# Kernel optimization log

Measured on AMD Instinct MI355X. Metric: run time of the kernel, lower is better.

Reference implementation:

```python
import jax, jax.numpy as jnp
import numpy as np

# Config mirrors TACO_hashed init: data_size=[1024,1024], dimensions=[[4]*5,[4]*5]
N = 262144          # number of query coordinates
DH = 256            # dim_hidden
TD = 4              # tile_dim = dimensions[0][0]
NLEV = 5            # n_levels
W0C = 30.0          # w0
DIMS = np.array([[4]*NLEV, [4]*NLEV])                 # [2, n_levels]
CUM = 1024 // np.cumprod(DIMS, axis=1)                # cum_bases per axis, [2, n_levels]


def setup_inputs() -> dict:
    key = jax.random.key(0)
    ks = jax.random.split(key, 9)
    s = 1.0 / np.sqrt(DH)
    e = TD * TD  # embedding dim = tile_dim**2 = 16
    return {
        "coords": jax.random.randint(ks[0], (N, 2), 0, 1024, dtype=jnp.int32),
        "W0": jax.random.normal(ks[1], (2, DH), jnp.float32) * (1.0 / np.sqrt(2.0)),
        "b0": jnp.zeros((DH,), jnp.float32),
        "Wh": jax.random.normal(ks[2], (3, DH, DH), jnp.float32) * s,  # hidden SIREN linears
        "bh": jnp.zeros((3, DH), jnp.float32),
        "emb": jax.random.normal(ks[3], (NLEV - 1, e, e), jnp.float32),      # per-level embedding tables
        "modW": jax.random.normal(ks[4], (NLEV - 1, e, DH), jnp.float32) * (1.0 / np.sqrt(e)),  # modulator linears (no bias)
        "Wl": jax.random.normal(ks[5], (DH, 3), jnp.float32) * s,  # last_layer
        "bl": jnp.zeros((3,), jnp.float32),
    }


def reference(coords, W0, b0, Wh, bh, emb, modW, Wl, bl):
    dims = jnp.asarray(DIMS.T)   # [n_levels, 2]
    cum = jnp.asarray(CUM.T)     # [n_levels, 2]
    # decompose_coords: per-level bitwise-style div/mod  -> [N, n_levels, 2]
    lv = (coords[:, None, :] // cum[None]) % dims[None]
    # modulator indices for levels 1..n_levels-1: idx = y*tile_dim + x  -> [N, n_levels-1]
    idx = lv[:, 1:, 1] * TD + lv[:, 1:, 0]
    # SIREN input is level-0 coords as float (faithful to the source)
    x = lv[:, 0, :].astype(jnp.float32) @ W0 + b0
    x = x + W0C * (emb[0][idx[:, 0]] @ modW[0])
    x = jnp.sin(W0C * x)
    for j in range(3):
        x = x @ Wh[j] + bh[j]
        x = x + W0C * (emb[j + 1][idx[:, j + 1]] @ modW[j + 1])
        x = jnp.sin(W0C * x)
    return x @ Wl + bl
```

## Files before the change

kernel.cpp:

```cpp
#include <hip/hip_runtime.h>
#include <hip/hip_bf16.h>
#include <math.h>


typedef float  f32x4  __attribute__((ext_vector_type(4)));
typedef int    i32x4  __attribute__((ext_vector_type(4)));
typedef __bf16 bf16x8 __attribute__((ext_vector_type(8)));

__device__ __forceinline__ float fbar(float v) {
  asm volatile("" : "+v"(v));
  return v;
}

__device__ __forceinline__ unsigned short f2bf_rne(float x) {
  unsigned u = __float_as_uint(x);
  unsigned r = (u + 0x7fffu + ((u >> 16) & 1u)) >> 16;
  return (unsigned short)r;
}

__device__ __forceinline__ void gload16(const void* g, void* l) {
  __builtin_amdgcn_global_load_lds(
      (const __attribute__((address_space(1))) unsigned*)g,
      (__attribute__((address_space(3))) unsigned*)l, 16, 0, 0);
}

__device__ __forceinline__ void sincos30(float x, float* so, float* co) {
  const float Ch = 4.774648189544678f;
  const float Cl = 1.0321218e-07f;
  float revh = x * Ch;
  fbar(revh);
  float e    = __builtin_fmaf(x, Ch, -revh);
  float revl = __builtin_fmaf(x, Cl, e);
  float k2   = __builtin_rintf(revh + revh);
  float g    = __builtin_fmaf(k2, -0.5f, revh) + revl;
  float u = g * g;
  float sr = -15.0946f;
  sr = __builtin_fmaf(sr, u, 42.0601f);
  sr = __builtin_fmaf(sr, u, -76.70585f);
  sr = __builtin_fmaf(sr, u, 81.6052492f);
  sr = __builtin_fmaf(sr, u, -41.341702f);
  sr = __builtin_fmaf(sr, u, 6.2831853f);
  float s = g * sr;
  float cr = -26.4259f;
  cr = __builtin_fmaf(cr, u, 60.2446f);
  cr = __builtin_fmaf(cr, u, -85.4568f);
  cr = __builtin_fmaf(cr, u, 64.9393940f);
  cr = __builtin_fmaf(cr, u, -19.7392088f);
  float c = __builtin_fmaf(cr, u, 1.0f);
  int ki = (int)k2;
  unsigned sgn = ((unsigned)(ki & 1)) << 31;
  *so = __uint_as_float(__float_as_uint(s) ^ sgn);
  *co = __uint_as_float(__float_as_uint(c) ^ sgn);
}

__global__ void k_prep(const float* __restrict__ emb, const float* __restrict__ modW,
                       float* __restrict__ Mf, float* __restrict__ T2C,
                       float* __restrict__ T2S, const float* __restrict__ Wl,
                       unsigned* __restrict__ B2u, const float* __restrict__ W2,
                       unsigned short* __restrict__ B2T) {
  int b = blockIdx.x, d = threadIdx.x;
  if (b < 64) {
    int j = b >> 4, i = b & 15;
    float acc = 0.0f;
#pragma unroll
    for (int e = 0; e < 16; ++e)
      acc = __builtin_fmaf(emb[j * 256 + i * 16 + e], modW[(j * 16 + e) * 256 + d], acc);
    Mf[b * 256 + d] = acc;
    if (j == 2) {
      float pm = fbar(30.0f * acc);
      float s, c;
      sincos30(pm, &s, &c);
      T2C[i * 256 + d] = c;
      T2S[i * 256 + d] = s;
    } else if (j == 3) {
      float pm = fbar(30.0f * acc);
      float s, c;
      sincos30(pm, &s, &c);
#pragma unroll
      for (int q = 0; q < 3; ++q) {
        float w = Wl[d * 3 + q];
        unsigned ts = (unsigned)f2bf_rne(s * w);
        unsigned tc = (unsigned)f2bf_rne(c * w);
        B2u[(i * 3 + q) * 256 + d] = (tc << 16) | ts;
      }
    }
  } else {
    int col = b - 64, k = d;
    float w = W2[k * 256 + col];
    unsigned short hi = f2bf_rne(w);
    float hif = __uint_as_float((unsigned)hi << 16);
    unsigned short lo = f2bf_rne(w - hif);
    B2T[col * 768 + k] = hi;
    B2T[col * 768 + 256 + k] = lo;
    B2T[col * 768 + 512 + k] = hi;
  }
}

__global__ void __launch_bounds__(512) k_h123(
    const float* __restrict__ W0, const float* __restrict__ b0,
    const float* __restrict__ Wh0, const float* __restrict__ bh0,
    const float* __restrict__ W1, const float* __restrict__ b1,
    const float* __restrict__ Mf, const float* __restrict__ T2C,
    const float* __restrict__ T2S,
    unsigned short* __restrict__ Ah, unsigned short* __restrict__ Al) {
  __shared__ float xs1[256];
  __shared__ float xs2[8][256];
  int b = blockIdx.x, t = threadIdx.x;
  int d = t & 255, hf = t >> 8;
  int c1 = b >> 1;
  int i1base = (b & 1) * 8 + hf * 4;
  if (hf == 0) {
    float lvx = (float)((c1 >> 6) & 3), lvy = (float)((c1 >> 4) & 3);
    int i0 = c1 & 15;
    float tt = fbar(lvx * W0[d]);
    tt = __builtin_fmaf(lvy, W0[256 + d], tt);
    tt = fbar(tt + b0[d]);
    float p = fbar(30.0f * Mf[i0 * 256 + d]);
    float xv = fbar(tt + p);
    xs1[d] = sinf(fbar(30.0f * xv));
  }
  __syncthreads();
  float acc = 0.0f;
  for (int k = 0; k < 256; ++k)
    acc = __builtin_fmaf(xs1[k], Wh0[k * 256 + d], acc);
  float t2 = fbar(acc + bh0[d]);
#pragma unroll
  for (int rr = 0; rr < 4; ++rr) {
    int i1 = i1base + rr;
    float pp = fbar(30.0f * Mf[4096 + i1 * 256 + d]);
    float x2 = fbar(t2 + pp);
    xs2[hf * 4 + rr][d] = sinf(fbar(30.0f * x2));
  }
  __syncthreads();
  float acc3[4] = {0.f, 0.f, 0.f, 0.f};
  for (int k = 0; k < 256; ++k) {
    float w = W1[k * 256 + d];
#pragma unroll
    for (int r = 0; r < 4; ++r)
      acc3[r] = __builtin_fmaf(xs2[hf * 4 + r][k], w, acc3[r]);
  }
  float tcv[16], tsv[16];
#pragma unroll
  for (int i = 0; i < 16; ++i) {
    tcv[i] = T2C[i * 256 + d];
    tsv[i] = T2S[i * 256 + d];
  }
  float bias = b1[d];
#pragma unroll
  for (int rr = 0; rr < 4; ++rr) {
    float targ = fbar(acc3[rr] + bias);
    float sT, cT;
    sincos30(targ, &sT, &cT);
    int c3base = (b * 8 + hf * 4 + rr) * 16;
#pragma unroll
    for (int i = 0; i < 16; ++i) {
      float hv = __builtin_fmaf(cT, tsv[i], sT * tcv[i]);
      unsigned short hi = f2bf_rne(hv);
      float hif = __uint_as_float((unsigned)hi << 16);
      unsigned short lo = f2bf_rne(hv - hif);
      size_t o = (size_t)(c3base + i) * 256 + d;
      Ah[o] = hi;
      Al[o] = lo;
    }
  }
}

__global__ void __launch_bounds__(512, 1) k_gemm(
    const unsigned short* __restrict__ Ah, const unsigned short* __restrict__ Al,
    const unsigned short* __restrict__ B2T, const float* __restrict__ b2,
    unsigned* __restrict__ SC) {
  __shared__ unsigned short As[2][128 * 32];
  __shared__ unsigned short Bs[2][256 * 32];
  const int t = threadIdx.x;
  const int lane = t & 63, wid = t >> 6;
  const int l15 = lane & 15, l4 = lane >> 4;
  const int wm = (wid >> 2) * 64;
  const int wn = (wid & 3) * 64;
  const size_t r0 = (size_t)blockIdx.x * 128;

  const int arow = t >> 2, apart = t & 3;
  const int gpart = (apart - ((arow >> 1) & 3)) & 3;
  const size_t bcol0 = t >> 2, bcol1 = (t >> 2) + 128;

  f32x4 acc[4][4];
#pragma unroll
  for (int rf = 0; rf < 4; ++rf)
#pragma unroll
    for (int cf = 0; cf < 4; ++cf) acc[rf][cf] = (f32x4){0.f, 0.f, 0.f, 0.f};

#define STAGE(c, bb)                                                         \
  {                                                                          \
    const unsigned short* asrc = ((c) >= 16) ? Al : Ah;                      \
    gload16(asrc + ((r0 + arow) << 8) + ((c) & 7) * 32 + gpart * 8,          \
            (void*)(&As[bb][wid * 512]));                                    \
    gload16(B2T + bcol0 * 768 + (c) * 32 + gpart * 8,                        \
            (void*)(&Bs[bb][wid * 512]));                                    \
    gload16(B2T + bcol1 * 768 + (c) * 32 + gpart * 8,                        \
            (void*)(&Bs[bb][(wid + 8) * 512]));                              \
  }

  STAGE(0, 0);
  __syncthreads();
  const int sp8 = ((l4 + (l15 >> 1)) & 3) * 8;
#pragma unroll 1
  for (int c = 0; c < 24; ++c) {
    int cur = c & 1;
    if (c < 23) STAGE(c + 1, cur ^ 1);
    bf16x8 af[4], bfr[4];
#pragma unroll
    for (int rf = 0; rf < 4; ++rf)
      af[rf] = __builtin_bit_cast(
          bf16x8, *(const i32x4*)(&As[cur][(wm + rf * 16 + l15) * 32 + sp8]));
#pragma unroll
    for (int cf = 0; cf < 4; ++cf)
      bfr[cf] = __builtin_bit_cast(
          bf16x8, *(const i32x4*)(&Bs[cur][(wn + cf * 16 + l15) * 32 + sp8]));
#pragma unroll
    for (int rf = 0; rf < 4; ++rf)
#pragma unroll
      for (int cf = 0; cf < 4; ++cf)
        acc[rf][cf] = __builtin_amdgcn_mfma_f32_16x16x32_bf16(
            af[rf], bfr[cf], acc[rf][cf], 0, 0, 0);
    __syncthreads();
  }
#undef STAGE

#pragma unroll
  for (int cf = 0; cf < 4; ++cf) {
    float bias = b2[wn + cf * 16 + l15];
#pragma unroll
    for (int rf = 0; rf < 4; ++rf) {
      size_t rbase = r0 + wm + rf * 16 + l4 * 4;
#pragma unroll
      for (int j = 0; j < 4; ++j) {
        float g = acc[rf][cf][j] + bias;
        float s, c;
        sincos30(g, &s, &c);
        unsigned pk = ((unsigned)f2bf_rne(s) << 16) | (unsigned)f2bf_rne(c);
        SC[(rbase + j) * 256 + wn + cf * 16 + l15] = pk;
      }
    }
  }
}

__global__ void __launch_bounds__(512, 1) k_ugemm(
    const unsigned short* __restrict__ SCb, const unsigned* __restrict__ B2u,
    float* __restrict__ U) {
  __shared__ unsigned short As[128 * 40];
  __shared__ unsigned Bs[48 * 260];
  const int t = threadIdx.x;
  const int lane = t & 63, wid = t >> 6;
  const int l15 = lane & 15, l4 = lane >> 4;
  const int wm = wid * 16;
  const size_t r0 = (size_t)blockIdx.x * 128;

#pragma unroll
  for (int i = 0; i < 24; ++i) {
    int lin = t + i * 512;
    int col = lin >> 8, kp = lin & 255;
    Bs[col * 260 + kp] = B2u[lin];
  }

  const int s_row = t >> 2, s_part = t & 3;
  f32x4 acc[3];
#pragma unroll
  for (int cf = 0; cf < 3; ++cf) acc[cf] = (f32x4){0.f, 0.f, 0.f, 0.f};

  i32x4 ra = *(const i32x4*)(SCb + (r0 + s_row) * 512 + s_part * 8);
#pragma unroll 1
  for (int c = 0; c < 16; ++c) {
    *(i32x4*)(As + s_row * 40 + s_part * 8) = ra;
    __syncthreads();
    if (c < 15)
      ra = *(const i32x4*)(SCb + (r0 + s_row) * 512 + (c + 1) * 32 + s_part * 8);
    bf16x8 af = __builtin_bit_cast(
        bf16x8, *(const i32x4*)(As + (wm + l15) * 40 + l4 * 8));
#pragma unroll
    for (int cf = 0; cf < 3; ++cf) {
      bf16x8 bfr = __builtin_bit_cast(
          bf16x8, *(const i32x4*)(Bs + (cf * 16 + l15) * 260 + c * 16 + l4 * 4));
      acc[cf] = __builtin_amdgcn_mfma_f32_16x16x32_bf16(af, bfr, acc[cf], 0, 0, 0);
    }
    __syncthreads();
  }

#pragma unroll
  for (int cf = 0; cf < 3; ++cf) {
    size_t rbase = r0 + wm + l4 * 4;
#pragma unroll
    for (int j = 0; j < 4; ++j)
      U[(rbase + j) * 48 + cf * 16 + l15] = acc[cf][j];
  }
}

__global__ void k_gather(const int* __restrict__ coords, const float* __restrict__ U,
                         const float* __restrict__ bl, float* __restrict__ out, int N) {
  int n = blockIdx.x * blockDim.x + threadIdx.x;
  if (n >= N) return;
  int x = coords[2 * n], y = coords[2 * n + 1];
  int c1 = ((x >> 8) & 3) * 64 + ((y >> 8) & 3) * 16 +
           (((y >> 6) & 3) * 4 + ((x >> 6) & 3));
  int i1 = ((y >> 4) & 3) * 4 + ((x >> 4) & 3);
  int i2 = ((y >> 2) & 3) * 4 + ((x >> 2) & 3);
  int i3 = (y & 3) * 4 + (x & 3);
  int c3 = (c1 * 16 + i1) * 16 + i2;
  const float* up = U + (size_t)c3 * 48 + i3 * 3;
  out[n * 3 + 0] = up[0] + bl[0];
  out[n * 3 + 1] = up[1] + bl[1];
  out[n * 3 + 2] = up[2] + bl[2];
}

__global__ void k_direct(const int* __restrict__ coords, const float* __restrict__ W0,
                         const float* __restrict__ b0, const float* __restrict__ Wh,
                         const float* __restrict__ bh, const float* __restrict__ emb,
                         const float* __restrict__ modW, const float* __restrict__ Wl,
                         const float* __restrict__ bl, float* __restrict__ out) {
  __shared__ float xs[256];
  __shared__ float red[256];
  int n = blockIdx.x, d = threadIdx.x;
  int x = coords[2 * n], y = coords[2 * n + 1];
  float lvx = (float)((x >> 8) & 3), lvy = (float)((y >> 8) & 3);
  int idx[4];
  idx[0] = ((y >> 6) & 3) * 4 + ((x >> 6) & 3);
  idx[1] = ((y >> 4) & 3) * 4 + ((x >> 4) & 3);
  idx[2] = ((y >> 2) & 3) * 4 + ((x >> 2) & 3);
  idx[3] = (y & 3) * 4 + (x & 3);
  float m = 0.0f;
#pragma unroll
  for (int e = 0; e < 16; ++e)
    m = __builtin_fmaf(emb[idx[0] * 16 + e], modW[e * 256 + d], m);
  float t = fbar(lvx * W0[d]);
  t = __builtin_fmaf(lvy, W0[256 + d], t);
  t = fbar(t + b0[d]);
  float p = fbar(30.0f * m);
  float xv = fbar(t + p);
  xs[d] = sinf(fbar(30.0f * xv));
  __syncthreads();
  for (int j = 0; j < 3; ++j) {
    float acc = 0.0f;
    for (int k = 0; k < 256; ++k)
      acc = __builtin_fmaf(xs[k], Wh[j * 65536 + k * 256 + d], acc);
    float tt = fbar(acc + bh[j * 256 + d]);
    m = 0.0f;
#pragma unroll
    for (int e = 0; e < 16; ++e)
      m = __builtin_fmaf(emb[(j + 1) * 256 + idx[j + 1] * 16 + e],
                         modW[((j + 1) * 16 + e) * 256 + d], m);
    p = fbar(30.0f * m);
    xv = fbar(tt + p);
    float h = sinf(fbar(30.0f * xv));
    __syncthreads();
    xs[d] = h;
    __syncthreads();
  }
  for (int q = 0; q < 3; ++q) {
    red[d] = xs[d] * Wl[d * 3 + q];
    __syncthreads();
    for (int s = 128; s > 0; s >>= 1) {
      if (d < s) red[d] += red[d + s];
      __syncthreads();
    }
    if (d == 0) out[n * 3 + q] = red[0] + bl[q];
    __syncthreads();
  }
}

extern "C" void kernel_launch(void* const* d_in, const int* in_sizes, int n_in,
                              void* d_out, int out_size, void* d_ws, size_t ws_size,
                              hipStream_t stream) {
  const int*   coords = (const int*)d_in[0];
  const float* W0   = (const float*)d_in[1];
  const float* b0   = (const float*)d_in[2];
  const float* Wh   = (const float*)d_in[3];
  const float* bh   = (const float*)d_in[4];
  const float* emb  = (const float*)d_in[5];
  const float* modW = (const float*)d_in[6];
  const float* Wl   = (const float*)d_in[7];
  const float* bl   = (const float*)d_in[8];
  float* out = (float*)d_out;
  const int N = in_sizes[0] / 2;

  const size_t OFF_MF  = 0;
  const size_t OFF_B2T = 65536;
  const size_t OFF_AH  = 458752;
  const size_t OFF_AL  = 34013184;
  const size_t OFF_SC  = 67567616;
  const size_t OFF_B2  = 134676480;
  const size_t OFF_T2C = 134774784;
  const size_t OFF_T2S = 134791168;
  const size_t OFF_U   = OFF_AH;
  const size_t NEED    = 134807552;

  if (ws_size >= NEED) {
    char* ws = (char*)d_ws;
    float*          Mf  = (float*)(ws + OFF_MF);
    unsigned short* B2T = (unsigned short*)(ws + OFF_B2T);
    unsigned short* Ahp = (unsigned short*)(ws + OFF_AH);
    unsigned short* Alp = (unsigned short*)(ws + OFF_AL);
    unsigned*       SC  = (unsigned*)(ws + OFF_SC);
    unsigned*       B2u = (unsigned*)(ws + OFF_B2);
    float*          T2C = (float*)(ws + OFF_T2C);
    float*          T2S = (float*)(ws + OFF_T2S);
    float*          U   = (float*)(ws + OFF_U);

    k_prep<<<320, 256, 0, stream>>>(emb, modW, Mf, T2C, T2S, Wl, B2u,
                                    Wh + 131072, B2T);
    k_h123<<<512, 512, 0, stream>>>(W0, b0, Wh, bh, Wh + 65536, bh + 256, Mf,
                                    T2C, T2S, Ahp, Alp);
    k_gemm<<<512, 512, 0, stream>>>(Ahp, Alp, B2T, bh + 512, SC);
    k_ugemm<<<512, 512, 0, stream>>>((const unsigned short*)SC, B2u, U);
    k_gather<<<(N + 255) / 256, 256, 0, stream>>>(coords, U, bl, out, N);
  } else {
    k_direct<<<N, 256, 0, stream>>>(coords, W0, b0, Wh, bh, emb, modW, Wl, bl, out);
  }
}
```

Measured before the change: 105.1 us.

## Retile k_gemm to 64-row blocks with vectorized SC stores and polynomial sin

The main GEMM moves from 128x256 tiles with 512 threads to 64x256 tiles with 256 threads and four blocks per CU, doubling the grid so more blocks can be resident for latency hiding. The epilogue now packs four column results into one 16-byte store, and B2u in k_prep is written with a permuted column order so the downstream ugemm reads match the new SC layout. The library sinf in k_h123 is replaced with a custom range-reduced polynomial. Each block now carries less A reuse per B tile load, and the permuted layout must stay consistent with how k_ugemm reads SC.

```diff
diff --git a/kernel.cpp b/kernel.cpp
--- a/kernel.cpp
+++ b/kernel.cpp
@@ -22,6 +22,27 @@
   __builtin_amdgcn_global_load_lds(
       (const __attribute__((address_space(1))) unsigned*)g,
       (__attribute__((address_space(3))) unsigned*)l, 16, 0, 0);
+}
+
+__device__ __forceinline__ float sin30(float x) {
+  const float Ch = 4.774648189544678f;
+  const float Cl = 1.0321218e-07f;
+  float revh = x * Ch;
+  fbar(revh);
+  float e    = __builtin_fmaf(x, Ch, -revh);
+  float revl = __builtin_fmaf(x, Cl, e);
+  float k2   = __builtin_rintf(revh + revh);
+  float g    = __builtin_fmaf(k2, -0.5f, revh) + revl;
+  float g2 = g * g;
+  float r = -15.0946f;
+  r = __builtin_fmaf(r, g2, 42.0601f);
+  r = __builtin_fmaf(r, g2, -76.70585f);
+  r = __builtin_fmaf(r, g2, 81.6052492f);
+  r = __builtin_fmaf(r, g2, -41.341702f);
+  r = __builtin_fmaf(r, g2, 6.2831853f);
+  float s = g * r;
+  int ki = (int)k2;
+  return __uint_as_float(__float_as_uint(s) ^ ((unsigned)(ki & 1) << 31));
 }
 
 __device__ __forceinline__ void sincos30(float x, float* so, float* co) {
@@ -76,12 +97,13 @@
       float pm = fbar(30.0f * acc);
       float s, c;
       sincos30(pm, &s, &c);
+      int p = (d & 0xC0) | ((d & 15) << 2) | ((d >> 4) & 3);
 #pragma unroll
       for (int q = 0; q < 3; ++q) {
         float w = Wl[d * 3 + q];
         unsigned ts = (unsigned)f2bf_rne(s * w);
         unsigned tc = (unsigned)f2bf_rne(c * w);
-        B2u[(i * 3 + q) * 256 + d] = (tc << 16) | ts;
+        B2u[(i * 3 + q) * 256 + p] = (tc << 16) | ts;
       }
     }
   } else {
@@ -129,7 +151,7 @@
     int i1 = i1base + rr;
     float pp = fbar(30.0f * Mf[4096 + i1 * 256 + d]);
     float x2 = fbar(t2 + pp);
-    xs2[hf * 4 + rr][d] = sinf(fbar(30.0f * x2));
+    xs2[hf * 4 + rr][d] = sin30(x2);
   }
   __syncthreads();
   float acc3[4] = {0.f, 0.f, 0.f, 0.f};
@@ -165,22 +187,20 @@
   }
 }
 
-__global__ void __launch_bounds__(512, 1) k_gemm(
+__global__ void __launch_bounds__(256, 4) k_gemm(
     const unsigned short* __restrict__ Ah, const unsigned short* __restrict__ Al,
     const unsigned short* __restrict__ B2T, const float* __restrict__ b2,
     unsigned* __restrict__ SC) {
-  __shared__ unsigned short As[2][128 * 32];
+  __shared__ unsigned short As[2][64 * 32];
   __shared__ unsigned short Bs[2][256 * 32];
   const int t = threadIdx.x;
   const int lane = t & 63, wid = t >> 6;
   const int l15 = lane & 15, l4 = lane >> 4;
-  const int wm = (wid >> 2) * 64;
-  const int wn = (wid & 3) * 64;
-  const size_t r0 = (size_t)blockIdx.x * 128;
+  const int wn = wid * 64;
+  const size_t r0 = (size_t)blockIdx.x * 64;
 
   const int arow = t >> 2, apart = t & 3;
   const int gpart = (apart - ((arow >> 1) & 3)) & 3;
-  const size_t bcol0 = t >> 2, bcol1 = (t >> 2) + 128;
 
   f32x4 acc[4][4];
 #pragma unroll
@@ -188,15 +208,15 @@
 #pragma unroll
     for (int cf = 0; cf < 4; ++cf) acc[rf][cf] = (f32x4){0.f, 0.f, 0.f, 0.f};
 
-#define STAGE(c, bb)                                                         \
-  {                                                                          \
-    const unsigned short* asrc = ((c) >= 16) ? Al : Ah;                      \
-    gload16(asrc + ((r0 + arow) << 8) + ((c) & 7) * 32 + gpart * 8,          \
-            (void*)(&As[bb][wid * 512]));                                    \
-    gload16(B2T + bcol0 * 768 + (c) * 32 + gpart * 8,                        \
-            (void*)(&Bs[bb][wid * 512]));                                    \
-    gload16(B2T + bcol1 * 768 + (c) * 32 + gpart * 8,                        \
-            (void*)(&Bs[bb][(wid + 8) * 512]));                              \
+#define STAGE(c, bb)                                                          \
+  {                                                                           \
+    const unsigned short* asrc = ((c) >= 16) ? Al : Ah;                       \
+    gload16(asrc + ((r0 + arow) << 8) + ((c) & 7) * 32 + gpart * 8,           \
+            (void*)(&As[bb][wid * 512]));                                     \
+    _Pragma("unroll")                                                         \
+    for (int x = 0; x < 4; ++x)                                               \
+      gload16(B2T + (size_t)(arow + 64 * x) * 768 + (c) * 32 + gpart * 8,     \
+              (void*)(&Bs[bb][(x * 4 + wid) * 512]));                         \
   }
 
   STAGE(0, 0);
@@ -210,7 +230,7 @@
 #pragma unroll
     for (int rf = 0; rf < 4; ++rf)
       af[rf] = __builtin_bit_cast(
-          bf16x8, *(const i32x4*)(&As[cur][(wm + rf * 16 + l15) * 32 + sp8]));
+          bf16x8, *(const i32x4*)(&As[cur][(rf * 16 + l15) * 32 + sp8]));
 #pragma unroll
     for (int cf = 0; cf < 4; ++cf)
       bfr[cf] = __builtin_bit_cast(
@@ -225,20 +245,24 @@
   }
 #undef STAGE
 
-#pragma unroll
-  for (int cf = 0; cf < 4; ++cf) {
-    float bias = b2[wn + cf * 16 + l15];
-#pragma unroll
-    for (int rf = 0; rf < 4; ++rf) {
-      size_t rbase = r0 + wm + rf * 16 + l4 * 4;
-#pragma unroll
-      for (int j = 0; j < 4; ++j) {
-        float g = acc[rf][cf][j] + bias;
+  float bias[4];
+#pragma unroll
+  for (int cf = 0; cf < 4; ++cf) bias[cf] = b2[wn + cf * 16 + l15];
+#pragma unroll
+  for (int rf = 0; rf < 4; ++rf) {
+#pragma unroll
+    for (int j = 0; j < 4; ++j) {
+      unsigned pk[4];
+#pragma unroll
+      for (int cf = 0; cf < 4; ++cf) {
+        float g = acc[rf][cf][j] + bias[cf];
         float s, c;
         sincos30(g, &s, &c);
-        unsigned pk = ((unsigned)f2bf_rne(s) << 16) | (unsigned)f2bf_rne(c);
-        SC[(rbase + j) * 256 + wn + cf * 16 + l15] = pk;
+        pk[cf] = ((unsigned)f2bf_rne(s) << 16) | (unsigned)f2bf_rne(c);
       }
+      size_t row = r0 + rf * 16 + l4 * 4 + j;
+      *(i32x4*)(SC + row * 256 + wn + l15 * 4) =
+          (i32x4){(int)pk[0], (int)pk[1], (int)pk[2], (int)pk[3]};
     }
   }
 }
@@ -407,7 +431,7 @@
                                     Wh + 131072, B2T);
     k_h123<<<512, 512, 0, stream>>>(W0, b0, Wh, bh, Wh + 65536, bh + 256, Mf,
                                     T2C, T2S, Ahp, Alp);
-    k_gemm<<<512, 512, 0, stream>>>(Ahp, Alp, B2T, bh + 512, SC);
+    k_gemm<<<1024, 256, 0, stream>>>(Ahp, Alp, B2T, bh + 512, SC);
     k_ugemm<<<512, 512, 0, stream>>>((const unsigned short*)SC, B2u, U);
     k_gather<<<(N + 255) / 256, 256, 0, stream>>>(coords, U, bl, out, N);
   } else {
```

Measured after the change: 117.0 us. 11.4% more time.
